# Performance work log

Measured on AMD Instinct MI355X. Metric: run time of the kernel, lower is better.

The kernel has to match this reference:

```python
import jax, jax.numpy as jnp
import numpy as np

B, S, D = 8, 2048, 512
E, DF = 16, 2048  # total experts, FFN hidden (4*d_model)
K = 4             # num_available_experts


def setup_inputs() -> dict:
    key = jax.random.key(0)
    ks = jax.random.split(key, 5)
    scale = 0.02
    return {
        "x": jax.random.normal(ks[0], (B, S, D), dtype=jnp.float32),
        "gate_w": jax.random.normal(ks[1], (E, D), dtype=jnp.float32) * scale,
        "gate_b": jnp.zeros((E,), dtype=jnp.float32),
        "w1": jax.random.normal(ks[2], (E, D, DF), dtype=jnp.float32) * scale,
        "b1": jnp.zeros((E, DF), dtype=jnp.float32),
        "w2": jax.random.normal(ks[3], (E, DF, D), dtype=jnp.float32) * scale,
        "b2": jnp.zeros((E, D), dtype=jnp.float32),
        "num_available": K,
    }


def reference(x, gate_w, gate_b, w1, b1, w2, b2, num_available):
    # Coarse expert selection: gate applied to the global token sum k = sum_{b,s} x
    k = jnp.sum(x, axis=(0, 1))                       # [D]
    coarse = gate_w @ k + gate_b                      # [E]
    _, idx = jax.lax.top_k(coarse, num_available)     # [K]

    # Gather selected experts' params
    gw_w, gw_b = gate_w[idx], gate_b[idx]             # [K,D], [K]
    W1, B1 = w1[idx], b1[idx]                         # [K,D,DF], [K,DF]
    W2, B2 = w2[idx], b2[idx]                         # [K,DF,D], [K,D]

    # Per-token softmax gating over the K selected experts
    logits = jnp.einsum('bsd,kd->bsk', x, gw_w) + gw_b  # [B,S,K]
    gw = jax.nn.softmax(logits, axis=2)                 # [B,S,K]

    # Dense expert FFNs over all tokens, weighted combine
    h = jax.nn.gelu(jnp.einsum('bsd,kdf->kbsf', x, W1) + B1[:, None, None, :])  # [K,B,S,DF]
    eo = jnp.einsum('kbsf,kfd->kbsd', h, W2) + B2[:, None, None, :]             # [K,B,S,D]
    out = jnp.einsum('kbsd,bsk->bsd', eo, gw)                                   # [B,S,D]
    return out
```

## Files before the change

### kernel.cpp

```cpp
#include <hip/hip_runtime.h>
#include <hip/hip_bf16.h>
#include <cstdint>
#include <cstddef>

typedef __attribute__((ext_vector_type(8))) short short8;
typedef __attribute__((ext_vector_type(4))) float f32x4;

#define AS1U32(p) ((const __attribute__((address_space(1))) uint32_t*)(p))
#define AS3U32(p) ((__attribute__((address_space(3))) uint32_t*)(p))

__device__ __forceinline__ unsigned short f2bf(float v) {
  union { float f; uint32_t u; } a; a.f = v;
  uint32_t u = a.u;
  u += 0x7FFFu + ((u >> 16) & 1u);
  return (unsigned short)(u >> 16);
}

__device__ __forceinline__ float gelu_fast(float x) {
  const float c0 = 0.7978845608028654f;
  const float c1 = 0.044715f;
  float u = c0 * (x + c1 * x * x * x);
  return x * __builtin_amdgcn_rcpf(1.0f + __expf(-2.0f * u));
}


__global__ __launch_bounds__(512)
void reduce_part(const float* __restrict__ x, float* __restrict__ kpart) {
  const int d = threadIdx.x;
  const int b = blockIdx.x;
  float s = 0.f;
#pragma unroll 4
  for (int i = 0; i < 64; i++)
    s += x[((size_t)b * 64 + i) * 512 + d];
  kpart[(size_t)b * 512 + d] = s;
}

__global__ __launch_bounds__(1024)
void gate_all(const float* __restrict__ kpart,
              const float* __restrict__ gate_w,
              const float* __restrict__ gate_b,
              const float* __restrict__ b1, const float* __restrict__ b2,
              int* __restrict__ idxout,
              float* __restrict__ b1cat, float* __restrict__ b2sel) {
  __shared__ float ksum2[2][512];
  __shared__ float coarse[16];
  __shared__ int idxl[4];
  const int t = threadIdx.x;
  {
    const int d = t & 511, h = t >> 9;
    float s = 0.f;
    for (int p = h * 128; p < h * 128 + 128; p++) s += kpart[(size_t)p * 512 + d];
    ksum2[h][d] = s;
  }
  __syncthreads();
  {
    const int wave = t >> 6, lane = t & 63;
    const int d0 = lane * 8;
    float s = 0.f;
#pragma unroll
    for (int j = 0; j < 8; j++)
      s += gate_w[wave * 512 + d0 + j] * (ksum2[0][d0 + j] + ksum2[1][d0 + j]);
#pragma unroll
    for (int off = 32; off >= 1; off >>= 1) s += __shfl_down(s, off, 64);
    if (lane == 0) coarse[wave] = s + gate_b[wave];
  }
  __syncthreads();
  if (t == 0) {
    unsigned taken = 0;
    for (int r = 0; r < 4; r++) {
      float best = -3.4e38f; int bi = 0;
      for (int e = 0; e < 16; e++)
        if (!((taken >> e) & 1u) && coarse[e] > best) { best = coarse[e]; bi = e; }
      taken |= 1u << bi;
      idxl[r] = bi; idxout[r] = bi;
    }
  }
  __syncthreads();
  for (int i = t; i < 8192; i += 1024)
    b1cat[i] = b1[(size_t)idxl[i >> 11] * 2048 + (i & 2047)];
  for (int i = t; i < 2048; i += 1024)
    b2sel[i] = b2[(size_t)idxl[i >> 9] * 512 + (i & 511)];
}

__global__ __launch_bounds__(256)
void transpose_all(const float* __restrict__ w1, const float* __restrict__ w2,
                   unsigned short* __restrict__ w1t, unsigned short* __restrict__ w2t,
                   const int* __restrict__ idx) {
  __shared__ float tl[64][65];
  const int tid = threadIdx.x;
  const int ty = tid >> 6, tx = tid & 63;
  const int z = blockIdx.z;
  const float* src; unsigned short* dbase; int C, dstLd, r0, c0;
  if (z < 4) {
    src = w1 + (size_t)idx[z] * 512 * 2048;
    dbase = w1t + (size_t)z * 2048 * 512;
    C = 2048; dstLd = 512;
    r0 = blockIdx.x * 64; c0 = blockIdx.y * 64;
  } else {
    src = w2 + (size_t)idx[z - 4] * 2048 * 512;
    dbase = w2t + (size_t)(z - 4) * 2048;
    C = 512; dstLd = 8192;
    r0 = blockIdx.y * 64; c0 = blockIdx.x * 64;
  }
#pragma unroll
  for (int i = 0; i < 16; i++) {
    int r = ty * 16 + i;
    tl[r][tx] = src[(size_t)(r0 + r) * C + c0 + tx];
  }
  __syncthreads();
#pragma unroll
  for (int i = 0; i < 16; i++) {
    int rr = ty * 16 + i;
    dbase[(size_t)(c0 + rr) * dstLd + r0 + tx] = f2bf(tl[tx][rr]);
  }
}

__global__ __launch_bounds__(256)
void gate_softmax_xconv(const float* __restrict__ x,
                        const float* __restrict__ gate_w,
                        const float* __restrict__ gate_b,
                        const int* __restrict__ idx,
                        float* __restrict__ gwout,
                        unsigned short* __restrict__ xbf) {
  __shared__ float wsel[4][512];
  __shared__ float bsel[4];
  const int tid = threadIdx.x;
  for (int i = tid; i < 2048; i += 256) {
    int k = i >> 9;
    wsel[k][i & 511] = gate_w[(size_t)idx[k] * 512 + (i & 511)];
  }
  if (tid < 4) bsel[tid] = gate_b[idx[tid]];
  __syncthreads();
  const int wave = tid >> 6, lane = tid & 63;
  const int t = blockIdx.x * 4 + wave;
  const float* xr = x + (size_t)t * 512 + lane * 8;
  float4 v0 = ((const float4*)xr)[0];
  float4 v1 = ((const float4*)xr)[1];
  float vals[8] = {v0.x, v0.y, v0.z, v0.w, v1.x, v1.y, v1.z, v1.w};
  short8 pk;
#pragma unroll
  for (int j = 0; j < 8; j++) pk[j] = (short)f2bf(vals[j]);
  *(short8*)(xbf + (size_t)t * 512 + lane * 8) = pk;
  float a0 = 0.f, a1 = 0.f, a2 = 0.f, a3 = 0.f;
  const int dbase = lane * 8;
#pragma unroll
  for (int j = 0; j < 8; j++) {
    float xv = vals[j];
    a0 += xv * wsel[0][dbase + j];
    a1 += xv * wsel[1][dbase + j];
    a2 += xv * wsel[2][dbase + j];
    a3 += xv * wsel[3][dbase + j];
  }
#pragma unroll
  for (int off = 32; off >= 1; off >>= 1) {
    a0 += __shfl_down(a0, off, 64);
    a1 += __shfl_down(a1, off, 64);
    a2 += __shfl_down(a2, off, 64);
    a3 += __shfl_down(a3, off, 64);
  }
  if (lane == 0) {
    float l0 = a0 + bsel[0], l1 = a1 + bsel[1], l2 = a2 + bsel[2], l3 = a3 + bsel[3];
    float m = fmaxf(fmaxf(l0, l1), fmaxf(l2, l3));
    float e0 = __expf(l0 - m), e1 = __expf(l1 - m);
    float e2 = __expf(l2 - m), e3 = __expf(l3 - m);
    float inv = 1.0f / (e0 + e1 + e2 + e3);
    float* o = gwout + (size_t)t * 4;
    o[0] = e0 * inv; o[1] = e1 * inv; o[2] = e2 * inv; o[3] = e3 * inv;
  }
}

template <int EPI>
__global__ __launch_bounds__(256, 2)
void gemm_bt(const unsigned short* __restrict__ A,
             const unsigned short* __restrict__ Bt,
             void* __restrict__ C, int K, int lda, int ldb, int ldc,
             const float* __restrict__ gw,
             const float* __restrict__ bias, int colOff, int accum) {
  __shared__ unsigned short lA[128 * 64];
  __shared__ unsigned short lB[128 * 64];
  const int tid = threadIdx.x;
  const int wave = tid >> 6;
  const int lane = tid & 63;
  const int rowA0 = blockIdx.x * 128;
  const int rowB0 = blockIdx.y * 128;

  f32x4 acc[4][4];
#pragma unroll
  for (int i = 0; i < 4; i++)
#pragma unroll
    for (int j = 0; j < 4; j++) acc[i][j] = (f32x4){0.f, 0.f, 0.f, 0.f};

  const int lrow = lane >> 3;
  const int lslot = lane & 7;
  const int gchunk = lslot ^ lrow;
  const int fr = lane & 15;
  const int quad = lane >> 4;
  const int wm = (wave >> 1) * 64;
  const int wn = (wave & 1) * 64;
  const int swz = fr & 7;

  for (int kt = 0; kt < K; kt += 64) {
#pragma unroll
    for (int c = 0; c < 4; c++) {
      int r = wave * 32 + c * 8 + lrow;
      const unsigned short* gp = A + (size_t)(rowA0 + r) * lda + kt + gchunk * 8;
      __builtin_amdgcn_global_load_lds(AS1U32(gp), AS3U32(lA + (wave * 32 + c * 8) * 64), 16, 0, 0);
    }
#pragma unroll
    for (int c = 0; c < 4; c++) {
      int r = wave * 32 + c * 8 + lrow;
      const unsigned short* gp = Bt + (size_t)(rowB0 + r) * ldb + kt + gchunk * 8;
      __builtin_amdgcn_global_load_lds(AS1U32(gp), AS3U32(lB + (wave * 32 + c * 8) * 64), 16, 0, 0);
    }
    __syncthreads();
#pragma unroll
    for (int ks = 0; ks < 2; ks++) {
      short8 af[4], bfr[4];
      const int c = ks * 4 + quad;
      const int slot = (c ^ swz) << 3;
#pragma unroll
      for (int i = 0; i < 4; i++)
        af[i] = *(const short8*)(lA + (wm + i * 16 + fr) * 64 + slot);
#pragma unroll
      for (int j = 0; j < 4; j++)
        bfr[j] = *(const short8*)(lB + (wn + j * 16 + fr) * 64 + slot);
#pragma unroll
      for (int i = 0; i < 4; i++)
#pragma unroll
        for (int j = 0; j < 4; j++)
          acc[i][j] = __builtin_amdgcn_mfma_f32_16x16x32_bf16(af[i], bfr[j], acc[i][j], 0, 0, 0);
    }
    __syncthreads();
  }

  if (EPI == 1) {
    unsigned short* Cb = (unsigned short*)C;
    const int kexp = (colOff + rowB0) >> 11;
#pragma unroll
    for (int i = 0; i < 4; i++) {
#pragma unroll
      for (int reg = 0; reg < 4; reg++) {
        int r = rowA0 + wm + i * 16 + quad * 4 + reg;
        float g = gw[(size_t)r * 4 + kexp];
#pragma unroll
        for (int j = 0; j < 4; j++) {
          int n = rowB0 + wn + j * 16 + fr;
          float v = acc[i][j][reg] + bias[colOff + n];
          Cb[(size_t)r * ldc + n] = f2bf(gelu_fast(v) * g);
        }
      }
    }
  } else {
    float* Cf = (float*)C;
#pragma unroll
    for (int i = 0; i < 4; i++) {
#pragma unroll
      for (int reg = 0; reg < 4; reg++) {
        int r = rowA0 + wm + i * 16 + quad * 4 + reg;
        size_t t4 = (size_t)r * 4;
        float g0 = gw[t4], g1 = gw[t4 + 1], g2 = gw[t4 + 2], g3 = gw[t4 + 3];
#pragma unroll
        for (int j = 0; j < 4; j++) {
          int n = rowB0 + wn + j * 16 + fr;
          size_t ci = (size_t)r * 512 + n;
          float v = acc[i][j][reg];
          if (accum) v += Cf[ci];
          else v += g0 * bias[n] + g1 * bias[512 + n] +
                    g2 * bias[1024 + n] + g3 * bias[1536 + n];
          Cf[ci] = v;
        }
      }
    }
  }
}


extern "C" void kernel_launch(void* const* d_in, const int* in_sizes, int n_in,
                              void* d_out, int out_size, void* d_ws, size_t ws_size,
                              hipStream_t stream) {
  (void)in_sizes; (void)n_in; (void)out_size;
  const float* x      = (const float*)d_in[0];
  const float* gate_w = (const float*)d_in[1];
  const float* gate_b = (const float*)d_in[2];
  const float* w1     = (const float*)d_in[3];
  const float* b1     = (const float*)d_in[4];
  const float* w2     = (const float*)d_in[5];
  const float* b2     = (const float*)d_in[6];

  char* ws = (char*)d_ws;
  int*            idx   = (int*)(ws + 0);
  float*          gw    = (float*)(ws + 4096);
  float*          b1cat = (float*)(ws + 266240);
  float*          b2sel = (float*)(ws + 299008);
  float*          kpart = (float*)(ws + 307200);
  unsigned short* xbf   = (unsigned short*)(ws + 831488);
  unsigned short* w1t   = (unsigned short*)(ws + 17608704);
  unsigned short* w2t   = (unsigned short*)(ws + 25997312);
  unsigned short* hbuf  = (unsigned short*)(ws + 34385920);
  const size_t HBUF_OFF = 34385920;

  size_t avail = ws_size > HBUF_OFF ? ws_size - HBUF_OFF : 0;
  int nslab = 1;
  while (nslab < 16 && (size_t)16384 * (8192 / nslab) * 2 > avail) nslab <<= 1;
  const int slabDF = 8192 / nslab;

  reduce_part<<<256, 512, 0, stream>>>(x, kpart);
  gate_all<<<1, 1024, 0, stream>>>(kpart, gate_w, gate_b, b1, b2, idx, b1cat, b2sel);
  transpose_all<<<dim3(8, 32, 8), 256, 0, stream>>>(w1, w2, w1t, w2t, idx);
  gate_softmax_xconv<<<4096, 256, 0, stream>>>(x, gate_w, gate_b, idx, gw, xbf);

  for (int s = 0; s < nslab; s++) {
    const int c0 = s * slabDF;
    gemm_bt<1><<<dim3(128, slabDF / 128), 256, 0, stream>>>(
        xbf, w1t + (size_t)c0 * 512, hbuf,
        512, 512, 512, slabDF,
        gw, b1cat, c0, 0);
    gemm_bt<2><<<dim3(128, 4), 256, 0, stream>>>(
        hbuf, w2t + c0, (float*)d_out,
        slabDF, slabDF, 8192, 512,
        gw, b2sel, 0, s > 0);
  }
}
```

Before: 529.0 us.

## Replace GEMM with 8-wave double-buffered pipelined kernel and larger tiles

Replaces the 128x128 single-buffered GEMM with an 8-wave, 256-row tile kernel that double-buffers LDS. It interleaves async global-to-LDS loads with MFMA phases under explicit waitcnt/barrier control and raises MFMA priority with setprio. The second GEMM gets XCD-aware block swizzling to improve L2 locality. The aim is to hide memory latency and increase data reuse per tile. The cost is more registers and LDS per block and a fragile hand-scheduled barrier sequence.

```diff
diff --git a/kernel.cpp b/kernel.cpp
--- a/kernel.cpp
+++ b/kernel.cpp
@@ -169,110 +169,203 @@
   }
 }
 
-template <int EPI>
-__global__ __launch_bounds__(256, 2)
-void gemm_bt(const unsigned short* __restrict__ A,
-             const unsigned short* __restrict__ Bt,
-             void* __restrict__ C, int K, int lda, int ldb, int ldc,
-             const float* __restrict__ gw,
-             const float* __restrict__ bias, int colOff, int accum) {
-  __shared__ unsigned short lA[128 * 64];
-  __shared__ unsigned short lB[128 * 64];
+
+#define CFENCE asm volatile("" ::: "memory")
+#define BAR    do { CFENCE; __builtin_amdgcn_s_barrier(); CFENCE; } while (0)
+#define LGKM0  do { asm volatile("s_waitcnt lgkmcnt(0)" ::: "memory"); \
+                    __builtin_amdgcn_sched_barrier(0); } while (0)
+#define VMW(n) asm volatile("s_waitcnt vmcnt(" #n ")" ::: "memory")
+
+#define LDA(abuf, mh)                                                       \
+  do {                                                                      \
+    _Pragma("unroll")                                                       \
+    for (int m_ = 0; m_ < 4; m_++)                                          \
+      _Pragma("unroll")                                                     \
+      for (int ks_ = 0; ks_ < 2; ks_++)                                     \
+        aF[m_][ks_] = *(const short8*)((abuf) +                             \
+            (size_t)(wr * 128 + ((mh) * 4 + m_) * 16 + fr) * 64 +           \
+            (((ks_ * 4 + quad) ^ swz) * 8));                                \
+  } while (0)
+
+#define LDB(bbuf, nh)                                                       \
+  do {                                                                      \
+    _Pragma("unroll")                                                       \
+    for (int n_ = 0; n_ < NF2; n_++)                                        \
+      _Pragma("unroll")                                                     \
+      for (int ks_ = 0; ks_ < 2; ks_++)                                     \
+        bF[nh][n_][ks_] = *(const short8*)((bbuf) +                         \
+            (size_t)(wc * NWV + ((nh) * NF2 + n_) * 16 + fr) * 64 +         \
+            (((ks_ * 4 + quad) ^ swz) * 8));                                \
+  } while (0)
+
+#define MM(mh, nh)                                                          \
+  do {                                                                      \
+    __builtin_amdgcn_s_setprio(1);                                          \
+    _Pragma("unroll")                                                       \
+    for (int m_ = 0; m_ < 4; m_++)                                          \
+      _Pragma("unroll")                                                     \
+      for (int n_ = 0; n_ < NF2; n_++)                                      \
+        _Pragma("unroll")                                                   \
+        for (int ks_ = 0; ks_ < 2; ks_++)                                   \
+          acc[(mh) * 4 + m_][(nh) * NF2 + n_] =                             \
+              __builtin_amdgcn_mfma_f32_16x16x32_bf16(                      \
+                  aF[m_][ks_], bF[nh][n_][ks_],                             \
+                  acc[(mh) * 4 + m_][(nh) * NF2 + n_], 0, 0, 0);            \
+    __builtin_amdgcn_s_setprio(0);                                          \
+  } while (0)
+
+template <int NFREP, int EPI>
+__global__ __launch_bounds__(512, 2)
+void gemm8p(const unsigned short* __restrict__ A,
+            const unsigned short* __restrict__ Bt,
+            void* __restrict__ C, int K, int lda, int ldb, int ldc,
+            const float* __restrict__ gw,
+            const float* __restrict__ bias, int colOff, int accum, int doswz) {
+  constexpr int BM = 256;
+  constexpr int BN = NFREP * 64;
+  constexpr int NWV = NFREP * 16;
+  constexpr int NF2 = NFREP / 2;
+  __shared__ unsigned short lds[2 * (BM * 64 + BN * 64)];
+
   const int tid = threadIdx.x;
-  const int wave = tid >> 6;
-  const int lane = tid & 63;
-  const int rowA0 = blockIdx.x * 128;
-  const int rowB0 = blockIdx.y * 128;
-
-  f32x4 acc[4][4];
-#pragma unroll
-  for (int i = 0; i < 4; i++)
-#pragma unroll
-    for (int j = 0; j < 4; j++) acc[i][j] = (f32x4){0.f, 0.f, 0.f, 0.f};
-
-  const int lrow = lane >> 3;
-  const int lslot = lane & 7;
-  const int gchunk = lslot ^ lrow;
-  const int fr = lane & 15;
-  const int quad = lane >> 4;
-  const int wm = (wave >> 1) * 64;
-  const int wn = (wave & 1) * 64;
-  const int swz = fr & 7;
-
-  for (int kt = 0; kt < K; kt += 64) {
-#pragma unroll
-    for (int c = 0; c < 4; c++) {
-      int r = wave * 32 + c * 8 + lrow;
-      const unsigned short* gp = A + (size_t)(rowA0 + r) * lda + kt + gchunk * 8;
-      __builtin_amdgcn_global_load_lds(AS1U32(gp), AS3U32(lA + (wave * 32 + c * 8) * 64), 16, 0, 0);
+  const int wave = tid >> 6, lane = tid & 63;
+  const int lrow = lane >> 3, lslot = lane & 7, gch = lslot ^ lrow;
+  const int wr = wave >> 2, wc = wave & 3;
+  const int fr = lane & 15, quad = lane >> 4, swz = fr & 7;
+
+  int bx = blockIdx.x, by = blockIdx.y;
+  if (doswz) {
+    int nwg = gridDim.x * gridDim.y;
+    int lin = by * gridDim.x + bx;
+    int sw = (lin & 7) * (nwg >> 3) + (lin >> 3);
+    bx = sw % gridDim.x; by = sw / gridDim.x;
+  }
+  const int rowA0 = bx * BM;
+  const int rowB0 = by * BN;
+
+  unsigned short* const A0 = lds;
+  unsigned short* const B0 = lds + BM * 64;
+  unsigned short* const A1 = lds + (BM * 64 + BN * 64);
+  unsigned short* const B1 = A1 + BM * 64;
+
+  auto stA = [&](unsigned short* ab, int h, int kt) {
+#pragma unroll
+    for (int j = 0; j < 2; j++) {
+      int rg = h * 8 + wave + j * 16;
+      const unsigned short* gp =
+          A + (size_t)(rowA0 + rg * 8 + lrow) * lda + kt + gch * 8;
+      __builtin_amdgcn_global_load_lds(AS1U32(gp), AS3U32(ab + rg * 512), 16, 0, 0);
     }
-#pragma unroll
-    for (int c = 0; c < 4; c++) {
-      int r = wave * 32 + c * 8 + lrow;
-      const unsigned short* gp = Bt + (size_t)(rowB0 + r) * ldb + kt + gchunk * 8;
-      __builtin_amdgcn_global_load_lds(AS1U32(gp), AS3U32(lB + (wave * 32 + c * 8) * 64), 16, 0, 0);
+  };
+  auto stB = [&](unsigned short* bb, int nh, int kt) {
+    if constexpr (NFREP == 4) {
+#pragma unroll
+      for (int j = 0; j < 2; j++) {
+        int idx = j * 8 + wave;
+        int rg = (idx >> 2) * 8 + (idx & 3) + nh * 4;
+        const unsigned short* gp =
+            Bt + (size_t)(rowB0 + rg * 8 + lrow) * ldb + kt + gch * 8;
+        __builtin_amdgcn_global_load_lds(AS1U32(gp), AS3U32(bb + rg * 512), 16, 0, 0);
+      }
+    } else {
+      int rg = (wave >> 1) * 4 + (wave & 1) + nh * 2;
+      const unsigned short* gp =
+          Bt + (size_t)(rowB0 + rg * 8 + lrow) * ldb + kt + gch * 8;
+      __builtin_amdgcn_global_load_lds(AS1U32(gp), AS3U32(bb + rg * 512), 16, 0, 0);
     }
-    __syncthreads();
-#pragma unroll
-    for (int ks = 0; ks < 2; ks++) {
-      short8 af[4], bfr[4];
-      const int c = ks * 4 + quad;
-      const int slot = (c ^ swz) << 3;
-#pragma unroll
-      for (int i = 0; i < 4; i++)
-        af[i] = *(const short8*)(lA + (wm + i * 16 + fr) * 64 + slot);
-#pragma unroll
-      for (int j = 0; j < 4; j++)
-        bfr[j] = *(const short8*)(lB + (wn + j * 16 + fr) * 64 + slot);
-#pragma unroll
-      for (int i = 0; i < 4; i++)
-#pragma unroll
-        for (int j = 0; j < 4; j++)
-          acc[i][j] = __builtin_amdgcn_mfma_f32_16x16x32_bf16(af[i], bfr[j], acc[i][j], 0, 0, 0);
-    }
-    __syncthreads();
-  }
+  };
+
+  f32x4 acc[8][NFREP];
+#pragma unroll
+  for (int i = 0; i < 8; i++)
+#pragma unroll
+    for (int j = 0; j < NFREP; j++) acc[i][j] = (f32x4){0.f, 0.f, 0.f, 0.f};
+
+  short8 aF[4][2];
+  short8 bF[2][NF2][2];
+
+  stB(B0, 0, 0); stB(B0, 1, 0); stA(A0, 0, 0); stA(A0, 1, 0);
+  stB(B1, 0, 64); stB(B1, 1, 64); stA(A1, 0, 64); stA(A1, 1, 64);
+  if constexpr (NFREP == 4) VMW(8); else VMW(6);
+  BAR;
+
+  const int niter = K >> 7;
+  for (int i = 0; i < niter - 1; i++) {
+    const int kt = i * 128;
+    LDA(A0, 0); LDB(B0, 0);
+    BAR; LGKM0; MM(0, 0); BAR;
+    LDB(B0, 1); stB(B0, 0, kt + 128);
+    BAR; LGKM0; MM(0, 1); BAR;
+    LDA(A0, 1); stB(B0, 1, kt + 128);
+    BAR; LGKM0; MM(1, 1); BAR;
+    stA(A0, 0, kt + 128);
+    BAR; LGKM0; MM(1, 0);
+    if constexpr (NFREP == 4) VMW(6); else VMW(4);
+    BAR;
+    LDA(A1, 0); LDB(B1, 0); stA(A0, 1, kt + 128);
+    BAR; LGKM0; MM(0, 0); BAR;
+    LDB(B1, 1); stB(B1, 0, kt + 192);
+    BAR; LGKM0; MM(0, 1); BAR;
+    LDA(A1, 1); stB(B1, 1, kt + 192);
+    BAR; LGKM0; MM(1, 1); BAR;
+    stA(A1, 0, kt + 192); stA(A1, 1, kt + 192);
+    BAR; LGKM0; MM(1, 0);
+    if constexpr (NFREP == 4) VMW(8); else VMW(6);
+    BAR;
+  }
+  LDA(A0, 0); LDB(B0, 0); BAR; LGKM0; MM(0, 0); BAR;
+  LDB(B0, 1);             BAR; LGKM0; MM(0, 1); BAR;
+  LDA(A0, 1);             BAR; LGKM0; MM(1, 1); BAR;
+                          BAR; LGKM0; MM(1, 0); VMW(0); BAR;
+  LDA(A1, 0); LDB(B1, 0); BAR; LGKM0; MM(0, 0); BAR;
+  LDB(B1, 1);             BAR; LGKM0; MM(0, 1); BAR;
+  LDA(A1, 1);             BAR; LGKM0; MM(1, 1); BAR;
+                          BAR; LGKM0; MM(1, 0);
 
   if (EPI == 1) {
     unsigned short* Cb = (unsigned short*)C;
     const int kexp = (colOff + rowB0) >> 11;
 #pragma unroll
-    for (int i = 0; i < 4; i++) {
+    for (int m = 0; m < 8; m++) {
 #pragma unroll
       for (int reg = 0; reg < 4; reg++) {
-        int r = rowA0 + wm + i * 16 + quad * 4 + reg;
+        int r = rowA0 + wr * 128 + m * 16 + quad * 4 + reg;
         float g = gw[(size_t)r * 4 + kexp];
 #pragma unroll
-        for (int j = 0; j < 4; j++) {
-          int n = rowB0 + wn + j * 16 + fr;
-          float v = acc[i][j][reg] + bias[colOff + n];
-          Cb[(size_t)r * ldc + n] = f2bf(gelu_fast(v) * g);
+        for (int n = 0; n < NFREP; n++) {
+          int col = rowB0 + wc * NWV + n * 16 + fr;
+          float v = acc[m][n][reg] + bias[colOff + col];
+          Cb[(size_t)r * ldc + col] = f2bf(gelu_fast(v) * g);
         }
       }
     }
   } else {
     float* Cf = (float*)C;
 #pragma unroll
-    for (int i = 0; i < 4; i++) {
+    for (int m = 0; m < 8; m++) {
 #pragma unroll
       for (int reg = 0; reg < 4; reg++) {
-        int r = rowA0 + wm + i * 16 + quad * 4 + reg;
+        int r = rowA0 + wr * 128 + m * 16 + quad * 4 + reg;
         size_t t4 = (size_t)r * 4;
         float g0 = gw[t4], g1 = gw[t4 + 1], g2 = gw[t4 + 2], g3 = gw[t4 + 3];
 #pragma unroll
-        for (int j = 0; j < 4; j++) {
-          int n = rowB0 + wn + j * 16 + fr;
-          size_t ci = (size_t)r * 512 + n;
-          float v = acc[i][j][reg];
+        for (int n = 0; n < NFREP; n++) {
+          int col = rowB0 + wc * NWV + n * 16 + fr;
+          size_t ci = (size_t)r * 512 + col;
+          float v = acc[m][n][reg];
           if (accum) v += Cf[ci];
-          else v += g0 * bias[n] + g1 * bias[512 + n] +
-                    g2 * bias[1024 + n] + g3 * bias[1536 + n];
+          else v += g0 * bias[col] + g1 * bias[512 + col] +
+                    g2 * bias[1024 + col] + g3 * bias[1536 + col];
           Cf[ci] = v;
         }
       }
     }
   }
 }
+
+#undef LDA
+#undef LDB
+#undef MM
 
 
 extern "C" void kernel_launch(void* const* d_in, const int* in_sizes, int n_in,
@@ -311,13 +404,13 @@
 
   for (int s = 0; s < nslab; s++) {
     const int c0 = s * slabDF;
-    gemm_bt<1><<<dim3(128, slabDF / 128), 256, 0, stream>>>(
+    gemm8p<4, 1><<<dim3(64, slabDF / 256), 512, 0, stream>>>(
         xbf, w1t + (size_t)c0 * 512, hbuf,
         512, 512, 512, slabDF,
-        gw, b1cat, c0, 0);
-    gemm_bt<2><<<dim3(128, 4), 256, 0, stream>>>(
+        gw, b1cat, c0, 0, 0);
+    gemm8p<2, 2><<<dim3(64, 4), 512, 0, stream>>>(
         hbuf, w2t + c0, (float*)d_out,
         slabDF, slabDF, 8192, 512,
-        gw, b2sel, 0, s > 0);
-  }
-}
+        gw, b2sel, 0, s > 0, 1);
+  }
+}
```

Result: slower. 559.3 us (+5.7%).

## Replace second expert GEMM with 256x128 double-buffered 8-wave pipelined kernel

Applied to the files above, without the earlier changes.

Adds a new GEMM kernel for the down-projection (hbuf x W2) that uses 256x128 tiles, 512 threads, and double-buffered LDS filled through direct global-to-LDS loads. Explicit barriers, waitcnts and priority bumps interleave the MFMA work on one half of the tile with prefetching the next tile. The aim is to hide memory latency and raise MFMA utilisation in the K=8192 GEMM. The trade-off is a larger LDS footprint and only 256 blocks in the grid, which can lower occupancy or leave parts of the GPU idle.

```diff
diff --git a/kernel.cpp b/kernel.cpp
--- a/kernel.cpp
+++ b/kernel.cpp
@@ -275,6 +275,149 @@
 }
 
 
+#define CFENCE asm volatile("" ::: "memory")
+#define BAR    do { CFENCE; __builtin_amdgcn_s_barrier(); CFENCE; } while (0)
+#define LGKM0  do { asm volatile("s_waitcnt lgkmcnt(0)" ::: "memory"); \
+                    __builtin_amdgcn_sched_barrier(0); } while (0)
+#define SCHEDB __builtin_amdgcn_sched_barrier(0)
+#define VMW(n) asm volatile("s_waitcnt vmcnt(" #n ")" ::: "memory")
+
+#define LDALL(abuf, bbuf)                                                   \
+  do {                                                                      \
+    _Pragma("unroll")                                                       \
+    for (int m_ = 0; m_ < 8; m_++)                                          \
+      _Pragma("unroll")                                                     \
+      for (int ks_ = 0; ks_ < 2; ks_++)                                     \
+        aF[m_][ks_] = *(const short8*)((abuf) +                             \
+            (size_t)(wr * 128 + m_ * 16 + fr) * 64 +                        \
+            (((ks_ * 4 + quad) ^ swz) * 8));                                \
+    _Pragma("unroll")                                                       \
+    for (int nh_ = 0; nh_ < 2; nh_++)                                       \
+      _Pragma("unroll")                                                     \
+      for (int ks_ = 0; ks_ < 2; ks_++)                                     \
+        bF[nh_][ks_] = *(const short8*)((bbuf) +                            \
+            (size_t)(wc * 32 + nh_ * 16 + fr) * 64 +                        \
+            (((ks_ * 4 + quad) ^ swz) * 8));                                \
+  } while (0)
+
+#define MMH(h)                                                              \
+  do {                                                                      \
+    __builtin_amdgcn_s_setprio(1);                                          \
+    _Pragma("unroll")                                                       \
+    for (int m_ = 0; m_ < 4; m_++)                                          \
+      _Pragma("unroll")                                                     \
+      for (int nh_ = 0; nh_ < 2; nh_++)                                     \
+        _Pragma("unroll")                                                   \
+        for (int ks_ = 0; ks_ < 2; ks_++)                                   \
+          acc[(h) * 4 + m_][nh_] =                                          \
+              __builtin_amdgcn_mfma_f32_16x16x32_bf16(                      \
+                  aF[(h) * 4 + m_][ks_], bF[nh_][ks_],                      \
+                  acc[(h) * 4 + m_][nh_], 0, 0, 0);                         \
+    __builtin_amdgcn_s_setprio(0);                                          \
+  } while (0)
+
+__global__ __launch_bounds__(512, 2)
+void gemm4p(const unsigned short* __restrict__ A,
+            const unsigned short* __restrict__ Bt,
+            float* __restrict__ Cf, int K, int lda, int ldb,
+            const float* __restrict__ gw,
+            const float* __restrict__ bias, int accum) {
+  constexpr int BM = 256;
+  constexpr int BN = 128;
+  __shared__ unsigned short lds[2 * (BM * 64 + BN * 64)];
+
+  const int tid = threadIdx.x;
+  const int wave = tid >> 6, lane = tid & 63;
+  const int lrow = lane >> 3, lslot = lane & 7, gch = lslot ^ lrow;
+  const int wr = wave >> 2, wc = wave & 3;
+  const int fr = lane & 15, quad = lane >> 4, swz = fr & 7;
+
+  const int rowA0 = blockIdx.x * BM;
+  const int rowB0 = blockIdx.y * BN;
+
+  unsigned short* const A0 = lds;
+  unsigned short* const B0 = lds + BM * 64;
+  unsigned short* const A1 = lds + (BM * 64 + BN * 64);
+  unsigned short* const B1 = A1 + BM * 64;
+
+  auto stA = [&](unsigned short* ab, int h, int kt) {
+#pragma unroll
+    for (int j = 0; j < 2; j++) {
+      int rg = h * 8 + wave + j * 16;
+      const unsigned short* gp =
+          A + (size_t)(rowA0 + rg * 8 + lrow) * lda + kt + gch * 8;
+      __builtin_amdgcn_global_load_lds(AS1U32(gp), AS3U32(ab + rg * 512), 16, 0, 0);
+    }
+  };
+  auto stB = [&](unsigned short* bb, int nh, int kt) {
+    int rg = (wave >> 1) * 4 + (wave & 1) + nh * 2;
+    const unsigned short* gp =
+        Bt + (size_t)(rowB0 + rg * 8 + lrow) * ldb + kt + gch * 8;
+    __builtin_amdgcn_global_load_lds(AS1U32(gp), AS3U32(bb + rg * 512), 16, 0, 0);
+  };
+  auto stTile = [&](unsigned short* ab, unsigned short* bb, int kt) {
+    stB(bb, 0, kt); stB(bb, 1, kt);
+    stA(ab, 0, kt); stA(ab, 1, kt);
+  };
+
+  f32x4 acc[8][2];
+#pragma unroll
+  for (int i = 0; i < 8; i++)
+#pragma unroll
+    for (int j = 0; j < 2; j++) acc[i][j] = (f32x4){0.f, 0.f, 0.f, 0.f};
+
+  short8 aF[8][2];
+  short8 bF[2][2];
+
+  stTile(A0, B0, 0);
+  stTile(A1, B1, 64);
+  VMW(6);
+  BAR;
+
+  const int niter = K >> 7;
+  for (int i = 0; i < niter - 1; i++) {
+    const int kt = i * 128;
+    LDALL(A0, B0);
+    BAR; LGKM0; MMH(0); BAR;
+    stTile(A0, B0, kt + 128); SCHEDB;
+    MMH(1); VMW(6); BAR;
+    LDALL(A1, B1);
+    BAR; LGKM0; MMH(0); BAR;
+    stTile(A1, B1, kt + 192); SCHEDB;
+    MMH(1); VMW(6); BAR;
+  }
+  LDALL(A0, B0);
+  BAR; LGKM0; MMH(0); BAR;
+  MMH(1); VMW(0); BAR;
+  LDALL(A1, B1);
+  BAR; LGKM0; MMH(0); BAR;
+  MMH(1);
+
+#pragma unroll
+  for (int m = 0; m < 8; m++) {
+#pragma unroll
+    for (int reg = 0; reg < 4; reg++) {
+      int r = rowA0 + wr * 128 + m * 16 + quad * 4 + reg;
+      size_t t4 = (size_t)r * 4;
+      float g0 = gw[t4], g1 = gw[t4 + 1], g2 = gw[t4 + 2], g3 = gw[t4 + 3];
+#pragma unroll
+      for (int n = 0; n < 2; n++) {
+        int col = rowB0 + wc * 32 + n * 16 + fr;
+        size_t ci = (size_t)r * 512 + col;
+        float v = acc[m][n][reg];
+        if (accum) v += Cf[ci];
+        else v += g0 * bias[col] + g1 * bias[512 + col] +
+                  g2 * bias[1024 + col] + g3 * bias[1536 + col];
+        Cf[ci] = v;
+      }
+    }
+  }
+}
+
+#undef LDALL
+#undef MMH
+
+
 extern "C" void kernel_launch(void* const* d_in, const int* in_sizes, int n_in,
                               void* d_out, int out_size, void* d_ws, size_t ws_size,
                               hipStream_t stream) {
@@ -315,9 +458,9 @@
         xbf, w1t + (size_t)c0 * 512, hbuf,
         512, 512, 512, slabDF,
         gw, b1cat, c0, 0);
-    gemm_bt<2><<<dim3(128, 4), 256, 0, stream>>>(
+    gemm4p<<<dim3(64, 4), 512, 0, stream>>>(
         hbuf, w2t + c0, (float*)d_out,
-        slabDF, slabDF, 8192, 512,
-        gw, b2sel, 0, s > 0);
-  }
-}
+        slabDF, slabDF, 8192,
+        gw, b2sel, s > 0);
+  }
+}
```

New measurement: 530.7 us. About the same (+0.3%).

## Double-buffer GEMM LDS tiles with explicit waitcnt scheduling and cheaper GELU

Applied to the files above, without the earlier changes.

Replaces the single-buffered GEMM main loop with a two-stage ping-pong LDS pipeline. The next K-tile is loaded asynchronously into the free buffer while MFMAs run on the current one, using explicit vmcnt/lgkmcnt waits, sched barriers and setprio, so global load latency is hidden behind compute. It also rewrites the tanh-GELU as a single exp2 of a folded polynomial to save epilogue ALU work. The cost is doubled LDS per block (64 KB), which may limit occupancy, plus more fragile hand scheduling that assumes K is a multiple of 128.

```diff
diff --git a/kernel.cpp b/kernel.cpp
--- a/kernel.cpp
+++ b/kernel.cpp
@@ -17,10 +17,12 @@
 }
 
 __device__ __forceinline__ float gelu_fast(float x) {
-  const float c0 = 0.7978845608028654f;
-  const float c1 = 0.044715f;
-  float u = c0 * (x + c1 * x * x * x);
-  return x * __builtin_amdgcn_rcpf(1.0f + __expf(-2.0f * u));
+  const float A = -2.302118142f;
+  const float B = -0.102943494f;
+  float x2 = x * x;
+  float t = x * __builtin_fmaf(B, x2, A);
+  float e = __builtin_amdgcn_exp2f(t);
+  return x * __builtin_amdgcn_rcpf(1.0f + e);
 }
 
 
@@ -169,69 +171,112 @@
   }
 }
 
+
+#define CFENCE asm volatile("" ::: "memory")
+#define BAR    do { CFENCE; __builtin_amdgcn_s_barrier(); CFENCE; } while (0)
+#define LGKM0  do { asm volatile("s_waitcnt lgkmcnt(0)" ::: "memory"); \
+                    __builtin_amdgcn_sched_barrier(0); } while (0)
+#define SCHEDB __builtin_amdgcn_sched_barrier(0)
+#define VMW(n) asm volatile("s_waitcnt vmcnt(" #n ")" ::: "memory")
+
+#define LDALL(abuf, bbuf)                                                   \
+  do {                                                                      \
+    _Pragma("unroll")                                                       \
+    for (int i_ = 0; i_ < 4; i_++)                                          \
+      _Pragma("unroll")                                                     \
+      for (int ks_ = 0; ks_ < 2; ks_++)                                     \
+        aF[i_][ks_] = *(const short8*)((abuf) +                             \
+            (size_t)(wm + i_ * 16 + fr) * 64 +                              \
+            (((ks_ * 4 + quad) ^ swz) << 3));                               \
+    _Pragma("unroll")                                                       \
+    for (int j_ = 0; j_ < 4; j_++)                                          \
+      _Pragma("unroll")                                                     \
+      for (int ks_ = 0; ks_ < 2; ks_++)                                     \
+        bF[j_][ks_] = *(const short8*)((bbuf) +                             \
+            (size_t)(wn + j_ * 16 + fr) * 64 +                              \
+            (((ks_ * 4 + quad) ^ swz) << 3));                               \
+  } while (0)
+
+#define MMH(ks)                                                             \
+  do {                                                                      \
+    __builtin_amdgcn_s_setprio(1);                                          \
+    _Pragma("unroll")                                                       \
+    for (int i_ = 0; i_ < 4; i_++)                                          \
+      _Pragma("unroll")                                                     \
+      for (int j_ = 0; j_ < 4; j_++)                                        \
+        acc[i_][j_] = __builtin_amdgcn_mfma_f32_16x16x32_bf16(              \
+            aF[i_][ks], bF[j_][ks], acc[i_][j_], 0, 0, 0);                  \
+    __builtin_amdgcn_s_setprio(0);                                          \
+  } while (0)
+
 template <int EPI>
 __global__ __launch_bounds__(256, 2)
-void gemm_bt(const unsigned short* __restrict__ A,
-             const unsigned short* __restrict__ Bt,
-             void* __restrict__ C, int K, int lda, int ldb, int ldc,
-             const float* __restrict__ gw,
-             const float* __restrict__ bias, int colOff, int accum) {
-  __shared__ unsigned short lA[128 * 64];
-  __shared__ unsigned short lB[128 * 64];
+void gemm4p(const unsigned short* __restrict__ A,
+            const unsigned short* __restrict__ Bt,
+            void* __restrict__ C, int K, int lda, int ldb, int ldc,
+            const float* __restrict__ gw,
+            const float* __restrict__ bias, int colOff, int accum) {
+  __shared__ unsigned short lds[4 * 128 * 64];
   const int tid = threadIdx.x;
-  const int wave = tid >> 6;
-  const int lane = tid & 63;
+  const int wave = tid >> 6, lane = tid & 63;
+  const int lrow = lane >> 3, lslot = lane & 7, gch = lslot ^ lrow;
+  const int fr = lane & 15, quad = lane >> 4, swz = fr & 7;
+  const int wm = (wave >> 1) * 64, wn = (wave & 1) * 64;
   const int rowA0 = blockIdx.x * 128;
   const int rowB0 = blockIdx.y * 128;
 
-  f32x4 acc[4][4];
-#pragma unroll
-  for (int i = 0; i < 4; i++)
-#pragma unroll
-    for (int j = 0; j < 4; j++) acc[i][j] = (f32x4){0.f, 0.f, 0.f, 0.f};
-
-  const int lrow = lane >> 3;
-  const int lslot = lane & 7;
-  const int gchunk = lslot ^ lrow;
-  const int fr = lane & 15;
-  const int quad = lane >> 4;
-  const int wm = (wave >> 1) * 64;
-  const int wn = (wave & 1) * 64;
-  const int swz = fr & 7;
-
-  for (int kt = 0; kt < K; kt += 64) {
+  unsigned short* const A0 = lds;
+  unsigned short* const B0 = lds + 128 * 64;
+  unsigned short* const A1 = lds + 2 * 128 * 64;
+  unsigned short* const B1 = lds + 3 * 128 * 64;
+
+  auto stT = [&](unsigned short* ab, unsigned short* bb, int kt) {
 #pragma unroll
     for (int c = 0; c < 4; c++) {
       int r = wave * 32 + c * 8 + lrow;
-      const unsigned short* gp = A + (size_t)(rowA0 + r) * lda + kt + gchunk * 8;
-      __builtin_amdgcn_global_load_lds(AS1U32(gp), AS3U32(lA + (wave * 32 + c * 8) * 64), 16, 0, 0);
+      const unsigned short* gp = A + (size_t)(rowA0 + r) * lda + kt + gch * 8;
+      __builtin_amdgcn_global_load_lds(AS1U32(gp), AS3U32(ab + (wave * 32 + c * 8) * 64), 16, 0, 0);
     }
 #pragma unroll
     for (int c = 0; c < 4; c++) {
       int r = wave * 32 + c * 8 + lrow;
-      const unsigned short* gp = Bt + (size_t)(rowB0 + r) * ldb + kt + gchunk * 8;
-      __builtin_amdgcn_global_load_lds(AS1U32(gp), AS3U32(lB + (wave * 32 + c * 8) * 64), 16, 0, 0);
-    }
-    __syncthreads();
-#pragma unroll
-    for (int ks = 0; ks < 2; ks++) {
-      short8 af[4], bfr[4];
-      const int c = ks * 4 + quad;
-      const int slot = (c ^ swz) << 3;
-#pragma unroll
-      for (int i = 0; i < 4; i++)
-        af[i] = *(const short8*)(lA + (wm + i * 16 + fr) * 64 + slot);
-#pragma unroll
-      for (int j = 0; j < 4; j++)
-        bfr[j] = *(const short8*)(lB + (wn + j * 16 + fr) * 64 + slot);
-#pragma unroll
-      for (int i = 0; i < 4; i++)
-#pragma unroll
-        for (int j = 0; j < 4; j++)
-          acc[i][j] = __builtin_amdgcn_mfma_f32_16x16x32_bf16(af[i], bfr[j], acc[i][j], 0, 0, 0);
-    }
-    __syncthreads();
-  }
+      const unsigned short* gp = Bt + (size_t)(rowB0 + r) * ldb + kt + gch * 8;
+      __builtin_amdgcn_global_load_lds(AS1U32(gp), AS3U32(bb + (wave * 32 + c * 8) * 64), 16, 0, 0);
+    }
+  };
+
+  f32x4 acc[4][4];
+#pragma unroll
+  for (int i = 0; i < 4; i++)
+#pragma unroll
+    for (int j = 0; j < 4; j++) acc[i][j] = (f32x4){0.f, 0.f, 0.f, 0.f};
+
+  short8 aF[4][2];
+  short8 bF[4][2];
+
+  stT(A0, B0, 0);
+  stT(A1, B1, 64);
+  VMW(8);
+  BAR;
+
+  const int niter = K >> 7;
+  for (int i = 0; i < niter - 1; i++) {
+    const int kt = i * 128;
+    LDALL(A0, B0);
+    BAR; LGKM0; MMH(0); BAR;
+    stT(A0, B0, kt + 128); SCHEDB;
+    MMH(1); VMW(8); BAR;
+    LDALL(A1, B1);
+    BAR; LGKM0; MMH(0); BAR;
+    stT(A1, B1, kt + 192); SCHEDB;
+    MMH(1); VMW(8); BAR;
+  }
+  LDALL(A0, B0);
+  BAR; LGKM0; MMH(0); BAR;
+  MMH(1); VMW(0); BAR;
+  LDALL(A1, B1);
+  BAR; LGKM0; MMH(0); BAR;
+  MMH(1);
 
   if (EPI == 1) {
     unsigned short* Cb = (unsigned short*)C;
@@ -273,6 +318,9 @@
     }
   }
 }
+
+#undef LDALL
+#undef MMH
 
 
 extern "C" void kernel_launch(void* const* d_in, const int* in_sizes, int n_in,
@@ -311,11 +359,11 @@
 
   for (int s = 0; s < nslab; s++) {
     const int c0 = s * slabDF;
-    gemm_bt<1><<<dim3(128, slabDF / 128), 256, 0, stream>>>(
+    gemm4p<1><<<dim3(128, slabDF / 128), 256, 0, stream>>>(
         xbf, w1t + (size_t)c0 * 512, hbuf,
         512, 512, 512, slabDF,
         gw, b1cat, c0, 0);
-    gemm_bt<2><<<dim3(128, 4), 256, 0, stream>>>(
+    gemm4p<2><<<dim3(128, 4), 256, 0, stream>>>(
         hbuf, w2t + c0, (float*)d_out,
         slabDF, slabDF, 8192, 512,
         gw, b2sel, 0, s > 0);
```

Measured after the change: 502.1 us. 5.1% less time.
